# Performance work log

Measured on AMD Instinct MI355X. Metric: run time of the kernel, lower is better.

Reference implementation:

```python
import jax, jax.numpy as jnp
import numpy as np

B = 16        # number of point clouds
N_PER = 2048  # points per cloud
K = 16        # knn neighbors
NUM_CLASSES = 40


def setup_inputs() -> dict:
    key = jax.random.key(0)
    ks = jax.random.split(key, 12)
    N = B * N_PER
    pos = jax.random.normal(ks[0], (N, 3), jnp.float32)
    normal = jax.random.normal(ks[1], (N, 3), jnp.float32)
    normal = normal / jnp.linalg.norm(normal, axis=1, keepdims=True)
    batch = jnp.arange(N, dtype=jnp.int32) // N_PER
    s = 0.1
    return {
        "pos": pos, "normal": normal, "batch": batch,
        # conv1 local_nn: Linear(4,32) -> ReLU -> Linear(32,32)
        "W1a": jax.random.normal(ks[2], (4, 32), jnp.float32) * s,
        "b1a": jnp.zeros((32,), jnp.float32),
        "W1b": jax.random.normal(ks[3], (32, 32), jnp.float32) * s,
        "b1b": jnp.zeros((32,), jnp.float32),
        # conv2 local_nn: Linear(36,32) -> ReLU -> Linear(32,32)
        "W2a": jax.random.normal(ks[4], (36, 32), jnp.float32) * s,
        "b2a": jnp.zeros((32,), jnp.float32),
        "W2b": jax.random.normal(ks[5], (32, 32), jnp.float32) * s,
        "b2b": jnp.zeros((32,), jnp.float32),
        # classifier: Linear(32, 40)
        "Wc": jax.random.normal(ks[6], (32, NUM_CLASSES), jnp.float32) * s,
        "bc": jnp.zeros((NUM_CLASSES,), jnp.float32),
    }


def _angle(v1, v2):
    cross = jnp.cross(v1, v2)
    return jnp.arctan2(jnp.linalg.norm(cross, axis=-1), jnp.sum(v1 * v2, axis=-1))


def _ppf(pos_i, pos_j, n_i, n_j):
    d = pos_j - pos_i
    return jnp.stack([
        jnp.linalg.norm(d, axis=-1),
        _angle(n_i, d),
        _angle(n_j, d),
        _angle(n_i, n_j),
    ], axis=-1)


def _mlp(x, Wa, ba, Wb, bb):
    return jax.nn.relu(x @ Wa + ba) @ Wb + bb


def reference(pos, normal, batch, W1a, b1a, W1b, b1b, W2a, b2a, W2b, b2b, Wc, bc):
    N = pos.shape[0]
    # --- knn_graph(k=16, loop=False) per cloud (equal-size clouds) ---
    p = pos.reshape(B, N_PER, 3)
    d2 = jnp.sum((p[:, :, None, :] - p[:, None, :, :]) ** 2, axis=-1)  # [B,n,n]
    d2 = jnp.where(jnp.eye(N_PER, dtype=bool), jnp.inf, d2)            # no self loop
    _, nbr = jax.lax.top_k(-d2, K)                                      # [B,n,K]
    nbr_g = (nbr + (jnp.arange(B) * N_PER)[:, None, None]).reshape(N, K)

    pos_j = pos[nbr_g]      # [N,K,3]
    n_j = normal[nbr_g]     # [N,K,3]
    ppf = _ppf(pos[:, None, :], pos_j, normal[:, None, :], n_j)  # [N,K,4]

    # conv1: message = PPF only (Linear(4,32)), max aggregation, relu
    h = jax.nn.relu(jnp.max(_mlp(ppf, W1a, b1a, W1b, b1b), axis=1))  # [N,32]
    # conv2: message = [h_j, ppf] (Linear(36,32)), max aggregation, relu
    msg2 = jnp.concatenate([h[nbr_g], ppf], axis=-1)                  # [N,K,36]
    h2 = jax.nn.relu(jnp.max(_mlp(msg2, W2a, b2a, W2b, b2b), axis=1))  # [N,32]

    # global max pool per cloud + classifier
    pooled = jnp.max(h2.reshape(B, N_PER, 32), axis=1)  # [B,32]
    return pooled @ Wc + bc
```

## Files before the change

### kernel.cpp

```cpp
#include <hip/hip_runtime.h>
#include <math.h>


#define NPER 2048
#define NCLOUD 16

#define OFF_NBR  (size_t)(0u)
#define OFF_PPF  (size_t)(2u << 20)
#define OFF_G    (size_t)(10u << 20)
#define OFF_POOL (size_t)(14u << 20)

__device__ __forceinline__ float med3(float a, float b, float c) {
    return __builtin_amdgcn_fmed3f(a, b, c);
}
__device__ __forceinline__ void cex(float& a, float& b) {
    const float lo = fminf(a, b), hi = fmaxf(a, b); a = lo; b = hi;
}
__device__ __forceinline__ void bmerge8(float (&v)[8]) {
#pragma unroll
    for (int i = 0; i < 4; ++i) cex(v[i], v[i + 4]);
#pragma unroll
    for (int b = 0; b < 8; b += 4)
#pragma unroll
        for (int i = 0; i < 2; ++i) cex(v[b + i], v[b + i + 2]);
#pragma unroll
    for (int b = 0; b < 8; b += 2) cex(v[b], v[b + 1]);
}
__device__ __forceinline__ void bmerge16(float (&v)[16]) {
#pragma unroll
    for (int i = 0; i < 8; ++i) cex(v[i], v[i + 8]);
#pragma unroll
    for (int b = 0; b < 16; b += 8)
#pragma unroll
        for (int i = 0; i < 4; ++i) cex(v[b + i], v[b + i + 4]);
#pragma unroll
    for (int b = 0; b < 16; b += 4)
#pragma unroll
        for (int i = 0; i < 2; ++i) cex(v[b + i], v[b + i + 2]);
#pragma unroll
    for (int b = 0; b < 16; b += 2) cex(v[b], v[b + 1]);
}

__device__ __forceinline__ float angf(float ax, float ay, float az,
                                      float bx, float by, float bz) {
    const float cx = ay * bz - az * by;
    const float cy = az * bx - ax * bz;
    const float cz = ax * by - ay * bx;
    const float cn = sqrtf(cx * cx + cy * cy + cz * cz);
    const float dt = ax * bx + ay * by + az * bz;
    return atan2f(cn, dt);
}

__global__ __launch_bounds__(256) void knn_conv1(const float* __restrict__ pos,
                                                 const float* __restrict__ nrm,
                                                 const float* __restrict__ W1a,
                                                 const float* __restrict__ b1a,
                                                 const float* __restrict__ W1b,
                                                 const float* __restrict__ b1b,
                                                 const float* __restrict__ W2a,
                                                 const float* __restrict__ b2a,
                                                 int* __restrict__ nbr,
                                                 float* __restrict__ ppf,
                                                 float* __restrict__ G) {
    const int tid = threadIdx.x;
    const int pl  = tid >> 4;
    const int sl  = tid & 15;
    const int gp  = blockIdx.x * 16 + pl;
    const int cloud = gp >> 11;
    const int lp  = gp & 2047;
    const int cbase = cloud * NPER;

    __shared__ float4 tile[2048];
    __shared__ int    hiL[16][40];
    __shared__ int    cnt[16];

    if (tid < 16) cnt[tid] = 0;

#pragma unroll
    for (int c = 0; c < 8; ++c) {
        const int idx = c * 256 + tid;
        const float x = pos[(cbase + idx) * 3 + 0];
        const float y = pos[(cbase + idx) * 3 + 1];
        const float z = pos[(cbase + idx) * 3 + 2];
        tile[idx] = make_float4(x, y, z, x * x + y * y + z * z);
    }
    __syncthreads();

    const float4 P  = tile[lp];
    const float pn2 = P.w;
    const float m2x = -2.f * P.x, m2y = -2.f * P.y, m2z = -2.f * P.z;

    float dl[4];
#pragma unroll
    for (int m = 0; m < 4; ++m) dl[m] = INFINITY;

#pragma unroll 4
    for (int jj = 0; jj < 128; ++jj) {
        const int cand = jj * 16 + sl;
        const float4 C = tile[cand];
        float s = fmaf(m2x, C.x, fmaf(m2y, C.y, fmaf(m2z, C.z, C.w)));
        s = (cand == lp) ? INFINITY : s;
        dl[3] = med3(dl[2], dl[3], s);
        dl[2] = med3(dl[1], dl[2], s);
        dl[1] = med3(dl[0], dl[1], s);
        dl[0] = fminf(dl[0], s);
    }

    float tau_s;
    {
        float v8[8];
#pragma unroll
        for (int i = 0; i < 4; ++i) v8[i] = dl[i];
#pragma unroll
        for (int i = 0; i < 4; ++i) v8[7 - i] = __shfl_xor(dl[i], 1);
        bmerge8(v8);
        float v[16];
#pragma unroll
        for (int i = 0; i < 8; ++i) v[i] = v8[i];
#pragma unroll
        for (int i = 0; i < 8; ++i) v[15 - i] = __shfl_xor(v8[i], 2);
        bmerge16(v);
        {
            float p[16];
#pragma unroll
            for (int i = 0; i < 16; ++i) p[i] = __shfl_xor(v[i], 4);
            float w[16];
#pragma unroll
            for (int i = 0; i < 16; ++i) w[i] = fminf(v[i], p[15 - i]);
            bmerge16(w);
#pragma unroll
            for (int i = 0; i < 16; ++i) v[i] = w[i];
        }
        {
            float p[16];
#pragma unroll
            for (int i = 0; i < 16; ++i) p[i] = __shfl_xor(v[i], 8);
            float t = -INFINITY;
#pragma unroll
            for (int i = 0; i < 16; ++i) t = fmaxf(t, fminf(v[i], p[15 - i]));
            tau_s = t;
        }
    }
    const float tsw = tau_s + 6e-5f * (1.f + pn2 + fabsf(tau_s + pn2));

#pragma unroll 4
    for (int jj = 0; jj < 128; ++jj) {
        const int cand = jj * 16 + sl;
        const float4 C = tile[cand];
        const float s = fmaf(m2x, C.x, fmaf(m2y, C.y, fmaf(m2z, C.z, C.w)));
        if (s <= tsw && cand != lp) {
            const int k = atomicAdd(&cnt[pl], 1);
            if (k < 40) hiL[pl][k] = cand;
        }
    }
    __syncthreads();

    if (tid < 16) {
        int n = cnt[tid];
        n = n > 40 ? 40 : n;
        if (n != 16) {
            const int myl = (blockIdx.x * 16 + tid) & 2047;
            const float4 Q = tile[myl];
            unsigned long long keys[16];
#pragma unroll
            for (int m = 0; m < 16; ++m) keys[m] = ~0ULL;
            for (int i = 0; i < n; ++i) {
                const int cand = hiL[tid][i];
                const float4 C = tile[cand];
                const float dx = __fsub_rn(Q.x, C.x);
                const float dy = __fsub_rn(Q.y, C.y);
                const float dz = __fsub_rn(Q.z, C.z);
                const float d2 = __fadd_rn(__fadd_rn(__fmul_rn(dx, dx),
                                                     __fmul_rn(dy, dy)),
                                           __fmul_rn(dz, dz));
                const unsigned long long key =
                    ((unsigned long long)__float_as_uint(d2) << 32) |
                    (unsigned int)cand;
                if (key < keys[15]) {
#pragma unroll
                    for (int m = 15; m >= 1; --m) {
                        const bool up   = key < keys[m - 1];
                        const bool here = key < keys[m];
                        keys[m] = up ? keys[m - 1] : (here ? key : keys[m]);
                    }
                    if (key < keys[0]) keys[0] = key;
                }
            }
#pragma unroll
            for (int m = 0; m < 16; ++m)
                hiL[tid][m] = (int)(unsigned int)(keys[m] & 0xFFFFFFFFu);
        }
    }
    __syncthreads();

    const float nix = nrm[gp * 3 + 0], niy = nrm[gp * 3 + 1], niz = nrm[gp * 3 + 2];
    float4 x;
    {
        const int jl = hiL[pl][sl];
        const int j  = cbase + jl;
        nbr[gp * 16 + sl] = j;
        const float4 C = tile[jl];
        const float njx = nrm[j * 3 + 0], njy = nrm[j * 3 + 1], njz = nrm[j * 3 + 2];
        const float dx = C.x - P.x, dy = C.y - P.y, dz = C.z - P.z;
        x.x = sqrtf(dx * dx + dy * dy + dz * dz);
        x.y = angf(nix, niy, niz, dx, dy, dz);
        x.z = angf(njx, njy, njz, dx, dy, dz);
        x.w = angf(nix, niy, niz, njx, njy, njz);
        ((float4*)ppf)[(size_t)gp * 16 + sl] = x;
    }

    float h1[32];
#pragma unroll
    for (int o = 0; o < 32; ++o) {
        h1[o] = fmaxf(fmaf(x.x, W1a[o],
                     fmaf(x.y, W1a[32 + o],
                     fmaf(x.z, W1a[64 + o],
                     fmaf(x.w, W1a[96 + o], b1a[o])))), 0.f);
    }

    float hr[32];
#pragma unroll 1
    for (int ob = 0; ob < 4; ++ob) {
        float acc[8];
#pragma unroll
        for (int u = 0; u < 8; ++u) acc[u] = b1b[ob * 8 + u];
#pragma unroll
        for (int hh = 0; hh < 32; ++hh) {
            const float hv = h1[hh];
#pragma unroll
            for (int u = 0; u < 8; ++u)
                acc[u] = fmaf(hv, W1b[hh * 32 + ob * 8 + u], acc[u]);
        }
#pragma unroll
        for (int u = 0; u < 8; ++u) {
            float v = acc[u];
            v = fmaxf(v, __shfl_xor(v, 1));
            v = fmaxf(v, __shfl_xor(v, 2));
            v = fmaxf(v, __shfl_xor(v, 4));
            v = fmaxf(v, __shfl_xor(v, 8));
            hr[ob * 8 + u] = fmaxf(v, 0.f);
        }
    }

    {
        const int c0 = sl * 2;
        float g0 = b2a[c0], g1 = b2a[c0 + 1];
#pragma unroll
        for (int k = 0; k < 32; ++k) {
            g0 = fmaf(hr[k], W2a[k * 32 + c0], g0);
            g1 = fmaf(hr[k], W2a[k * 32 + c0 + 1], g1);
        }
        ((float2*)(G + (size_t)gp * 32))[sl] = make_float2(g0, g1);
    }
}

__global__ __launch_bounds__(256, 4) void conv2_pool(const float* __restrict__ ppf,
                                                     const int* __restrict__ nbr,
                                                     const float* __restrict__ G,
                                                     const float* __restrict__ W2a,
                                                     const float* __restrict__ W2b,
                                                     const float* __restrict__ b2b,
                                                     int* __restrict__ pooledi) {
    const int tid    = threadIdx.x;
    const int gid    = blockIdx.x * 256 + tid;
    const int node16 = tid >> 4;
    const int cloud  = blockIdx.x >> 7;

    const int j = nbr[gid];

    float h1[32];
    {
        const float4* gr = (const float4*)(G + (size_t)j * 32);
#pragma unroll
        for (int q = 0; q < 8; ++q) {
            const float4 v = gr[q];
            h1[q * 4 + 0] = v.x; h1[q * 4 + 1] = v.y;
            h1[q * 4 + 2] = v.z; h1[q * 4 + 3] = v.w;
        }
    }
    const float4 x = ((const float4*)ppf)[gid];
#pragma unroll
    for (int o = 0; o < 32; ++o) {
        h1[o] = fmaxf(fmaf(x.x, W2a[32 * 32 + o],
                     fmaf(x.y, W2a[33 * 32 + o],
                     fmaf(x.z, W2a[34 * 32 + o],
                     fmaf(x.w, W2a[35 * 32 + o], h1[o])))), 0.f);
    }

    float h2r[32];
#pragma unroll 1
    for (int ob = 0; ob < 4; ++ob) {
        float acc[8];
#pragma unroll
        for (int u = 0; u < 8; ++u) acc[u] = b2b[ob * 8 + u];
#pragma unroll
        for (int hh = 0; hh < 32; ++hh) {
            const float hv = h1[hh];
#pragma unroll
            for (int u = 0; u < 8; ++u)
                acc[u] = fmaf(hv, W2b[hh * 32 + ob * 8 + u], acc[u]);
        }
#pragma unroll
        for (int u = 0; u < 8; ++u) {
            float v = acc[u];
            v = fmaxf(v, __shfl_xor(v, 1));
            v = fmaxf(v, __shfl_xor(v, 2));
            v = fmaxf(v, __shfl_xor(v, 4));
            v = fmaxf(v, __shfl_xor(v, 8));
            h2r[ob * 8 + u] = fmaxf(v, 0.f);
        }
    }

    __shared__ float sh[16][33];
    if ((tid & 15) == 0) {
#pragma unroll
        for (int o = 0; o < 32; ++o) sh[node16][o] = h2r[o];
    }
    __syncthreads();
    if (tid < 32) {
        float m = sh[0][tid];
#pragma unroll
        for (int n = 1; n < 16; ++n) m = fmaxf(m, sh[n][tid]);
        atomicMax(&pooledi[cloud * 32 + tid], __float_as_int(m));
    }
}

__global__ __launch_bounds__(64) void fc_kernel(const int* __restrict__ pooledi,
                                                const float* __restrict__ Wc,
                                                const float* __restrict__ bc,
                                                float* __restrict__ out) {
    const int b = blockIdx.x;
    const int tid = threadIdx.x;
    if (tid < 40) {
        float acc = bc[tid];
#pragma unroll
        for (int o = 0; o < 32; ++o)
            acc = fmaf(__int_as_float(pooledi[b * 32 + o]), Wc[o * 40 + tid], acc);
        out[b * 40 + tid] = acc;
    }
}

extern "C" void kernel_launch(void* const* d_in, const int* in_sizes, int n_in,
                              void* d_out, int out_size, void* d_ws, size_t ws_size,
                              hipStream_t stream) {
    const float* pos = (const float*)d_in[0];
    const float* nrm = (const float*)d_in[1];
    const float* W1a = (const float*)d_in[3];
    const float* b1a = (const float*)d_in[4];
    const float* W1b = (const float*)d_in[5];
    const float* b1b = (const float*)d_in[6];
    const float* W2a = (const float*)d_in[7];
    const float* b2a = (const float*)d_in[8];
    const float* W2b = (const float*)d_in[9];
    const float* b2b = (const float*)d_in[10];
    const float* Wc  = (const float*)d_in[11];
    const float* bc  = (const float*)d_in[12];
    float* out = (float*)d_out;

    char* ws = (char*)d_ws;
    int*   nbr = (int*)(ws + OFF_NBR);
    float* ppf = (float*)(ws + OFF_PPF);
    float* G   = (float*)(ws + OFF_G);
    int*   pli = (int*)(ws + OFF_POOL);

    hipLaunchKernelGGL(knn_conv1,  dim3(2048), dim3(256), 0, stream,
                       pos, nrm, W1a, b1a, W1b, b1b, W2a, b2a, nbr, ppf, G);
    hipLaunchKernelGGL(conv2_pool, dim3(2048), dim3(256), 0, stream,
                       ppf, nbr, G, W2a, W2b, b2b, pli);
    hipLaunchKernelGGL(fc_kernel,  dim3(16),   dim3(64),  0, stream,
                       pli, Wc, bc, out);
}
```

Measured before the change: 193.6 us.

## Use polynomial atan2, 512-thread knn blocks, short neighbor lists, higher occupancy

Replaces atan2f in the point-pair-feature angles with a minimax polynomial approximation that uses a hardware reciprocal. The knn/conv1 kernel now handles 32 points per 512-thread block, so each shared-memory tile load of the cloud is amortized over twice as many queries, and the candidate list is stored as 16-bit indices to save LDS. conv2_pool raises its occupancy hint and writes the per-node max directly to shared memory instead of keeping a 32-float register array. The approximate atan2 trades a little accuracy for fewer instructions, and the higher occupancy bounds may force register spills.

```diff
diff --git a/kernel.cpp b/kernel.cpp
--- a/kernel.cpp
+++ b/kernel.cpp
@@ -39,6 +39,25 @@
         for (int i = 0; i < 2; ++i) cex(v[b + i], v[b + i + 2]);
 #pragma unroll
     for (int b = 0; b < 16; b += 2) cex(v[b], v[b + 1]);
+}
+
+__device__ __forceinline__ float fast_atan2p(float y, float x) {
+    const float ax = fabsf(x);
+    const float mn = fminf(ax, y), mx = fmaxf(ax, y);
+    float a = mn * __builtin_amdgcn_rcpf(mx);
+    a = (mx == 0.f) ? 0.f : a;
+    const float t = a * a;
+    float p = fmaf(t, 0.0028662257f, -0.0161657367f);
+    p = fmaf(t, p, 0.0429096138f);
+    p = fmaf(t, p, -0.0752896400f);
+    p = fmaf(t, p, 0.1065626393f);
+    p = fmaf(t, p, -0.1420889944f);
+    p = fmaf(t, p, 0.1999355085f);
+    p = fmaf(t, p, -0.3333314528f);
+    float r = fmaf(a * t, p, a);
+    r = (y > ax) ? (1.5707963268f - r) : r;
+    r = (x < 0.f) ? (3.1415926536f - r) : r;
+    return r;
 }
 
 __device__ __forceinline__ float angf(float ax, float ay, float az,
@@ -48,37 +67,37 @@
     const float cz = ax * by - ay * bx;
     const float cn = sqrtf(cx * cx + cy * cy + cz * cz);
     const float dt = ax * bx + ay * by + az * bz;
-    return atan2f(cn, dt);
-}
-
-__global__ __launch_bounds__(256) void knn_conv1(const float* __restrict__ pos,
-                                                 const float* __restrict__ nrm,
-                                                 const float* __restrict__ W1a,
-                                                 const float* __restrict__ b1a,
-                                                 const float* __restrict__ W1b,
-                                                 const float* __restrict__ b1b,
-                                                 const float* __restrict__ W2a,
-                                                 const float* __restrict__ b2a,
-                                                 int* __restrict__ nbr,
-                                                 float* __restrict__ ppf,
-                                                 float* __restrict__ G) {
+    return fast_atan2p(cn, dt);
+}
+
+__global__ __launch_bounds__(512, 8) void knn_conv1(const float* __restrict__ pos,
+                                                    const float* __restrict__ nrm,
+                                                    const float* __restrict__ W1a,
+                                                    const float* __restrict__ b1a,
+                                                    const float* __restrict__ W1b,
+                                                    const float* __restrict__ b1b,
+                                                    const float* __restrict__ W2a,
+                                                    const float* __restrict__ b2a,
+                                                    int* __restrict__ nbr,
+                                                    float* __restrict__ ppf,
+                                                    float* __restrict__ G) {
     const int tid = threadIdx.x;
     const int pl  = tid >> 4;
     const int sl  = tid & 15;
-    const int gp  = blockIdx.x * 16 + pl;
+    const int gp  = blockIdx.x * 32 + pl;
     const int cloud = gp >> 11;
     const int lp  = gp & 2047;
     const int cbase = cloud * NPER;
 
     __shared__ float4 tile[2048];
-    __shared__ int    hiL[16][40];
-    __shared__ int    cnt[16];
-
-    if (tid < 16) cnt[tid] = 0;
-
-#pragma unroll
-    for (int c = 0; c < 8; ++c) {
-        const int idx = c * 256 + tid;
+    __shared__ unsigned short hiL[32][40];
+    __shared__ int cnt[32];
+
+    if (tid < 32) cnt[tid] = 0;
+
+#pragma unroll
+    for (int c = 0; c < 4; ++c) {
+        const int idx = c * 512 + tid;
         const float x = pos[(cbase + idx) * 3 + 0];
         const float y = pos[(cbase + idx) * 3 + 1];
         const float z = pos[(cbase + idx) * 3 + 2];
@@ -150,16 +169,16 @@
         const float s = fmaf(m2x, C.x, fmaf(m2y, C.y, fmaf(m2z, C.z, C.w)));
         if (s <= tsw && cand != lp) {
             const int k = atomicAdd(&cnt[pl], 1);
-            if (k < 40) hiL[pl][k] = cand;
+            if (k < 40) hiL[pl][k] = (unsigned short)cand;
         }
     }
     __syncthreads();
 
-    if (tid < 16) {
+    if (tid < 32) {
         int n = cnt[tid];
         n = n > 40 ? 40 : n;
         if (n != 16) {
-            const int myl = (blockIdx.x * 16 + tid) & 2047;
+            const int myl = (blockIdx.x * 32 + tid) & 2047;
             const float4 Q = tile[myl];
             unsigned long long keys[16];
 #pragma unroll
@@ -188,7 +207,7 @@
             }
 #pragma unroll
             for (int m = 0; m < 16; ++m)
-                hiL[tid][m] = (int)(unsigned int)(keys[m] & 0xFFFFFFFFu);
+                hiL[tid][m] = (unsigned short)(keys[m] & 0xFFFFu);
         }
     }
     __syncthreads();
@@ -254,7 +273,7 @@
     }
 }
 
-__global__ __launch_bounds__(256, 4) void conv2_pool(const float* __restrict__ ppf,
+__global__ __launch_bounds__(256, 8) void conv2_pool(const float* __restrict__ ppf,
                                                      const int* __restrict__ nbr,
                                                      const float* __restrict__ G,
                                                      const float* __restrict__ W2a,
@@ -287,7 +306,7 @@
                      fmaf(x.w, W2a[35 * 32 + o], h1[o])))), 0.f);
     }
 
-    float h2r[32];
+    __shared__ float sh[16][33];
 #pragma unroll 1
     for (int ob = 0; ob < 4; ++ob) {
         float acc[8];
@@ -307,16 +326,11 @@
             v = fmaxf(v, __shfl_xor(v, 2));
             v = fmaxf(v, __shfl_xor(v, 4));
             v = fmaxf(v, __shfl_xor(v, 8));
-            h2r[ob * 8 + u] = fmaxf(v, 0.f);
-        }
-    }
-
-    __shared__ float sh[16][33];
-    if ((tid & 15) == 0) {
-#pragma unroll
-        for (int o = 0; o < 32; ++o) sh[node16][o] = h2r[o];
+            if ((tid & 15) == 0) sh[node16][ob * 8 + u] = fmaxf(v, 0.f);
+        }
     }
     __syncthreads();
+
     if (tid < 32) {
         float m = sh[0][tid];
 #pragma unroll
@@ -363,7 +377,7 @@
     float* G   = (float*)(ws + OFF_G);
     int*   pli = (int*)(ws + OFF_POOL);
 
-    hipLaunchKernelGGL(knn_conv1,  dim3(2048), dim3(256), 0, stream,
+    hipLaunchKernelGGL(knn_conv1,  dim3(1024), dim3(512), 0, stream,
                        pos, nrm, W1a, b1a, W1b, b1b, W2a, b2a, nbr, ppf, G);
     hipLaunchKernelGGL(conv2_pool, dim3(2048), dim3(256), 0, stream,
                        ppf, nbr, G, W2a, W2b, b2b, pli);
```

Measured after the change: 282.4 us. 1.46x slower.
